# Performance work log

Measured on AMD Instinct MI355X. Metric: run time of the kernel, lower is better.

The kernel has to match this reference:

```python
import jax, jax.numpy as jnp
import numpy as np

DIM = 768
HEADS = 12
HEAD_DIM = DIM // HEADS
SCALE = HEAD_DIM ** -0.5


def setup_inputs() -> dict:
    key = jax.random.key(0)
    k_x, k_qkv, k_ow, k_ob = jax.random.split(key, 4)
    B, N = 8, 1024
    x = jax.random.normal(k_x, (B, N, DIM), dtype=jnp.float32)
    # nn.Linear weights: out = x @ W.T + b; store torch-layout [out, in]
    w_qkv = jax.random.normal(k_qkv, (3 * DIM, DIM), dtype=jnp.float32) * (DIM ** -0.5)
    w_out = jax.random.normal(k_ow, (DIM, DIM), dtype=jnp.float32) * (DIM ** -0.5)
    b_out = jax.random.normal(k_ob, (DIM,), dtype=jnp.float32) * 0.01
    return {"x": x, "w_qkv": w_qkv, "w_out": w_out, "b_out": b_out}


def reference(x, w_qkv, w_out, b_out):
    B, N, C = x.shape
    qkv = jnp.einsum('bnc,dc->bnd', x, w_qkv)            # [B, N, 3C]
    qkv = qkv.reshape(B, N, 3, HEADS, HEAD_DIM)
    qkv = jnp.transpose(qkv, (2, 0, 3, 1, 4))            # [3, B, H, N, Dh]
    q, k, v = qkv[0], qkv[1], qkv[2]
    attn = jnp.einsum('bhqd,bhkd->bhqk', q, k) * SCALE   # [B, H, N, N]
    attn = jax.nn.softmax(attn, axis=-1)
    o = jnp.einsum('bhqk,bhkd->bhqd', attn, v)           # [B, H, N, Dh]
    o = jnp.transpose(o, (0, 2, 1, 3)).reshape(B, N, C)
    return jnp.einsum('bnc,dc->bnd', o, w_out) + b_out
```

## Files before the change

### kernel.cpp

```cpp
#include <hip/hip_runtime.h>

#define B_ 8
#define N_ 1024
#define DIM_ 768
#define H_ 12
#define DH_ 64
#define M_ (B_ * N_)
#define NQKV_ (3 * DIM_)
#define SCL_ 0.18033688011112042f

typedef unsigned short u16;
typedef unsigned int u32;
typedef __attribute__((ext_vector_type(8))) unsigned short u16x8;
typedef __attribute__((ext_vector_type(4))) unsigned short u16x4;
typedef __attribute__((ext_vector_type(8))) short bf16x8;
typedef __attribute__((ext_vector_type(4))) float f32x4;

__device__ __forceinline__ u16 f2bf(float f) {
  u32 u = __builtin_bit_cast(u32, f);
  u += 0x7fffu + ((u >> 16) & 1u);
  return (u16)(u >> 16);
}
__device__ __forceinline__ float bf2f(u16 v) {
  u32 u = ((u32)v) << 16;
  return __builtin_bit_cast(float, u);
}
__device__ __forceinline__ void async16(const void* g, void* l) {
  __builtin_amdgcn_global_load_lds(
      (const __attribute__((address_space(1))) unsigned int*)g,
      (__attribute__((address_space(3))) unsigned int*)l, 16, 0, 0);
}

__global__ __launch_bounds__(256) void cast_bf16_k(const float* __restrict__ in,
                                                   u16* __restrict__ out, int n4) {
  int i = blockIdx.x * 256 + threadIdx.x;
  if (i >= n4) return;
  float4 v = reinterpret_cast<const float4*>(in)[i];
  u16x4 o;
  o.x = f2bf(v.x); o.y = f2bf(v.y); o.z = f2bf(v.z); o.w = f2bf(v.w);
  reinterpret_cast<u16x4*>(out)[i] = o;
}

template <bool OUT_BF16, bool BIAS, bool VSPLIT>
__global__ __launch_bounds__(256) void gemm_bt_k(
    const u16* __restrict__ A, const u16* __restrict__ Bm,
    void* __restrict__ Cv, const float* __restrict__ bias, int K, int ldc,
    u16* __restrict__ vT) {
  __shared__ u16 As[128 * 32];
  __shared__ u16 Bs[128 * 32];
  const int t = threadIdx.x;
  const int lane = t & 63;
  const int wid = t >> 6;
  const int brow = blockIdx.y << 7;
  const int bcol = blockIdx.x << 7;
  const int wrow = (wid >> 1) << 6;
  const int wcol = (wid & 1) << 6;

  f32x4 acc[4][4];
#pragma unroll
  for (int m = 0; m < 4; ++m)
#pragma unroll
    for (int n = 0; n < 4; ++n) acc[m][n] = (f32x4){0.f, 0.f, 0.f, 0.f};

  const int loff0 = t << 4, loff1 = (t + 256) << 4;
  const int r0 = loff0 >> 6, r1 = loff1 >> 6;
  const int s0 = ((((loff0 >> 4) & 3) ^ (r0 & 3)) << 3);
  const int s1 = ((((loff1 >> 4) & 3) ^ (r1 & 3)) << 3);
  const u16* gA0 = A + (size_t)(brow + r0) * K + s0;
  const u16* gA1 = A + (size_t)(brow + r1) * K + s1;
  const u16* gB0 = Bm + (size_t)(bcol + r0) * K + s0;
  const u16* gB1 = Bm + (size_t)(bcol + r1) * K + s1;
  char* lA = (char*)As;
  char* lB = (char*)Bs;

  const int kb = (lane >> 4) << 4;
  int aoff[4], boff[4];
#pragma unroll
  for (int m = 0; m < 4; ++m) {
    int ra = wrow + (m << 4) + (lane & 15);
    aoff[m] = (ra << 6) + (kb ^ ((ra & 3) << 4));
    int rb = wcol + (m << 4) + (lane & 15);
    boff[m] = (rb << 6) + (kb ^ ((rb & 3) << 4));
  }

  const int nkt = K >> 5;
  for (int kt = 0; kt < nkt; ++kt) {
    const int ko = kt << 5;
    async16(gA0 + ko, lA + loff0);
    async16(gA1 + ko, lA + loff1);
    async16(gB0 + ko, lB + loff0);
    async16(gB1 + ko, lB + loff1);
    __syncthreads();
    bf16x8 af[4], bfr[4];
#pragma unroll
    for (int m = 0; m < 4; ++m) af[m] = *(const bf16x8*)(lA + aoff[m]);
#pragma unroll
    for (int n = 0; n < 4; ++n) bfr[n] = *(const bf16x8*)(lB + boff[n]);
#pragma unroll
    for (int m = 0; m < 4; ++m)
#pragma unroll
      for (int n = 0; n < 4; ++n)
        acc[m][n] = __builtin_amdgcn_mfma_f32_16x16x32_bf16(af[m], bfr[n],
                                                            acc[m][n], 0, 0, 0);
    __syncthreads();
  }

  const int crow = brow + wrow + ((lane >> 4) << 2);
  const int ccol0 = bcol + wcol + (lane & 15);
  if (VSPLIT && bcol >= 2 * DIM_) {
#pragma unroll
    for (int n = 0; n < 4; ++n) {
      int colh = ccol0 + (n << 4) - 2 * DIM_;
      int h = colh >> 6, d = colh & 63;
#pragma unroll
      for (int m = 0; m < 4; ++m) {
        int row0 = crow + (m << 4);
        int bb = row0 >> 10, nn = row0 & 1023;
        int hbl = bb * H_ + h;
        uint2 pk;
        pk.x = (u32)f2bf(acc[m][n][0]) | ((u32)f2bf(acc[m][n][1]) << 16);
        pk.y = (u32)f2bf(acc[m][n][2]) | ((u32)f2bf(acc[m][n][3]) << 16);
        *(uint2*)(vT + (((size_t)(hbl * 64 + d)) << 10) + nn) = pk;
      }
    }
    return;
  }
#pragma unroll
  for (int m = 0; m < 4; ++m)
#pragma unroll
    for (int n = 0; n < 4; ++n) {
      int col = ccol0 + (n << 4);
      float bv = BIAS ? bias[col] : 0.f;
#pragma unroll
      for (int j = 0; j < 4; ++j) {
        int row = crow + (m << 4) + j;
        if (OUT_BF16)
          ((u16*)Cv)[(size_t)row * ldc + col] = f2bf(acc[m][n][j]);
        else
          ((float*)Cv)[(size_t)row * ldc + col] = acc[m][n][j] + bv;
      }
    }
}

__global__ __launch_bounds__(256) void attn_k(const u16* __restrict__ qkv,
                                              const u16* __restrict__ vT,
                                              u16* __restrict__ ob) {
  __shared__ u16 Ks[64 * 64];
  __shared__ u16 Vt[64 * 64];
  __shared__ u16 Ps[4][16 * 64];
  const int t = threadIdx.x;
  const int lane = t & 63;
  const int w = t >> 6;
  const int g = lane >> 4;
  const int q15 = lane & 15;

  const int orig = blockIdx.x;
  const int sub = orig >> 3;
  const int hb = (orig & 7) * 12 + (sub >> 4);
  const int qt = sub & 15;
  const int b = hb / H_;
  const int h = hb - b * H_;
  const int rowbase = b * N_;
  const int qcol = h * DH_;
  const int kcol = DIM_ + qcol;

  bf16x8 qf[2];
  {
    const int qrow = rowbase + (qt << 6) + (w << 4) + q15;
    const u16* src = qkv + (size_t)qrow * NQKV_ + qcol + (g << 3);
#pragma unroll
    for (int ks = 0; ks < 2; ++ks) {
      u16x8 raw = *(const u16x8*)(src + ks * 32);
      bf16x8 o;
#pragma unroll
      for (int j = 0; j < 8; ++j) o[j] = (short)f2bf(bf2f(raw[j]) * SCL_);
      qf[ks] = o;
    }
  }

  float mrow = -1e30f, lrow = 0.f;
  f32x4 oacc[4];
#pragma unroll
  for (int d = 0; d < 4; ++d) oacc[d] = (f32x4){0.f, 0.f, 0.f, 0.f};

  const int sr = t >> 3;
  const int c8 = t & 7;
  const int loff0 = t << 4, loff1 = (t + 256) << 4;
  const u16* kg0 = qkv + (size_t)(rowbase + sr) * NQKV_ + kcol + ((c8 ^ (sr & 7)) << 3);
  const u16* kg1 = qkv + (size_t)(rowbase + sr + 32) * NQKV_ + kcol + ((c8 ^ (sr & 7)) << 3);
  const u16* vg0 = vT + (((size_t)(hb * 64 + sr)) << 10) + ((c8 ^ (sr & 7)) << 3);
  const u16* vg1 = vT + (((size_t)(hb * 64 + sr + 32)) << 10) + ((c8 ^ (sr & 7)) << 3);
  char* lk = (char*)Ks;
  char* lv = (char*)Vt;
  char* lp = (char*)&Ps[w][0];

  for (int kv = 0; kv < 16; ++kv) {
    __syncthreads();
    async16(kg0 + (size_t)kv * 64 * NQKV_, lk + loff0);
    async16(kg1 + (size_t)kv * 64 * NQKV_, lk + loff1);
    async16(vg0 + kv * 64, lv + loff0);
    async16(vg1 + kv * 64, lv + loff1);
    __syncthreads();

    f32x4 s[4];
#pragma unroll
    for (int n = 0; n < 4; ++n) s[n] = (f32x4){0.f, 0.f, 0.f, 0.f};
#pragma unroll
    for (int n = 0; n < 4; ++n) {
      int rk = (n << 4) + q15;
#pragma unroll
      for (int ks = 0; ks < 2; ++ks) {
        int off = (rk << 7) + (((ks << 6) + (g << 4)) ^ ((rk & 7) << 4));
        bf16x8 kf = *(const bf16x8*)(lk + off);
        s[n] = __builtin_amdgcn_mfma_f32_16x16x32_bf16(kf, qf[ks], s[n], 0, 0, 0);
      }
    }

    float mx = s[0][0];
#pragma unroll
    for (int n = 0; n < 4; ++n)
#pragma unroll
      for (int j = 0; j < 4; ++j) mx = fmaxf(mx, s[n][j]);
    mx = fmaxf(mx, __shfl_xor(mx, 16, 64));
    mx = fmaxf(mx, __shfl_xor(mx, 32, 64));
    float mn = fmaxf(mrow, mx);
    float al = exp2f(mrow - mn);
    mrow = mn;
    float p[4][4];
    float ps = 0.f;
#pragma unroll
    for (int n = 0; n < 4; ++n)
#pragma unroll
      for (int j = 0; j < 4; ++j) {
        p[n][j] = exp2f(s[n][j] - mn);
        ps += p[n][j];
      }
    ps += __shfl_xor(ps, 16, 64);
    ps += __shfl_xor(ps, 32, 64);
    lrow = lrow * al + ps;

    float alj[4];
#pragma unroll
    for (int j = 0; j < 4; ++j) alj[j] = __shfl(al, (g << 2) + j, 64);
#pragma unroll
    for (int d = 0; d < 4; ++d)
#pragma unroll
      for (int j = 0; j < 4; ++j) oacc[d][j] *= alj[j];

#pragma unroll
    for (int n = 0; n < 4; ++n) {
      uint2 pk;
      pk.x = (u32)f2bf(p[n][0]) | ((u32)f2bf(p[n][1]) << 16);
      pk.y = (u32)f2bf(p[n][2]) | ((u32)f2bf(p[n][3]) << 16);
      *(uint2*)(lp + (q15 << 7) + (((n << 5) + (g << 3)) ^ ((q15 & 7) << 4))) = pk;
    }

    bf16x8 pf[2];
#pragma unroll
    for (int ks = 0; ks < 2; ++ks)
      pf[ks] = *(const bf16x8*)(lp + (q15 << 7) +
                                (((ks << 6) + (g << 4)) ^ ((q15 & 7) << 4)));
#pragma unroll
    for (int dt = 0; dt < 4; ++dt) {
      int d = (dt << 4) + q15;
#pragma unroll
      for (int ks = 0; ks < 2; ++ks) {
        bf16x8 vf = *(const bf16x8*)(lv + (d << 7) +
                                     (((ks << 6) + (g << 4)) ^ ((d & 7) << 4)));
        oacc[dt] = __builtin_amdgcn_mfma_f32_16x16x32_bf16(pf[ks], vf, oacc[dt], 0, 0, 0);
      }
    }
  }

  float rl = 1.f / lrow;
  float rlj[4];
#pragma unroll
  for (int j = 0; j < 4; ++j) rlj[j] = __shfl(rl, (g << 2) + j, 64);
  const int orow0 = rowbase + (qt << 6) + (w << 4) + (g << 2);
#pragma unroll
  for (int dt = 0; dt < 4; ++dt) {
    int col = qcol + (dt << 4) + q15;
#pragma unroll
    for (int j = 0; j < 4; ++j)
      ob[(size_t)(orow0 + j) * DIM_ + col] = f2bf(oacc[dt][j] * rlj[j]);
  }
}

extern "C" void kernel_launch(void* const* d_in, const int* in_sizes, int n_in,
                              void* d_out, int out_size, void* d_ws, size_t ws_size,
                              hipStream_t stream) {
  const float* x = (const float*)d_in[0];
  const float* w_qkv = (const float*)d_in[1];
  const float* w_out = (const float*)d_in[2];
  const float* b_out = (const float*)d_in[3];

  u16* xb = (u16*)d_ws;
  u16* wqkvb = xb + (size_t)M_ * DIM_;
  u16* woutb = wqkvb + (size_t)NQKV_ * DIM_;
  u16* qkvb = woutb + (size_t)DIM_ * DIM_;
  u16* obuf = qkvb + (size_t)M_ * NQKV_;
  u16* vT = obuf + (size_t)M_ * DIM_;

  {
    int n4 = M_ * DIM_ / 4;
    cast_bf16_k<<<(n4 + 255) / 256, 256, 0, stream>>>(x, xb, n4);
  }
  {
    int n4 = NQKV_ * DIM_ / 4;
    cast_bf16_k<<<(n4 + 255) / 256, 256, 0, stream>>>(w_qkv, wqkvb, n4);
  }
  {
    int n4 = DIM_ * DIM_ / 4;
    cast_bf16_k<<<(n4 + 255) / 256, 256, 0, stream>>>(w_out, woutb, n4);
  }

  gemm_bt_k<true, false, true><<<dim3(NQKV_ / 128, M_ / 128), 256, 0, stream>>>(
      xb, wqkvb, (void*)qkvb, nullptr, DIM_, NQKV_, vT);

  attn_k<<<dim3(B_ * H_ * 16), 256, 0, stream>>>(qkvb, vT, obuf);

  gemm_bt_k<false, true, false><<<dim3(DIM_ / 128, M_ / 128), 256, 0, stream>>>(
      obuf, woutb, d_out, b_out, DIM_, DIM_, nullptr);
}
```

Baseline: 228.7 us.

## Double-buffer K/V tiles in attention and add lazy softmax rescaling

The attention kernel now double-buffers the K and V tiles in LDS, issuing the async loads for tile kv+1 before computing on tile kv so global latency overlaps with MFMA work. One barrier per iteration replaces the previous two. It also skips the online-softmax rescale of the accumulator unless the running max grows by more than 8 (log2 domain), and switches to the raw exp2 builtin, packed bf16 conversion and s_setprio hints around MFMA blocks. The costs are doubled LDS for K/V, which may lower occupancy, and that probabilities can reach up to 2^8 before rescaling, which changes rounding slightly.

```diff
diff --git a/kernel.cpp b/kernel.cpp
--- a/kernel.cpp
+++ b/kernel.cpp
@@ -24,6 +24,11 @@
 __device__ __forceinline__ float bf2f(u16 v) {
   u32 u = ((u32)v) << 16;
   return __builtin_bit_cast(float, u);
+}
+__device__ __forceinline__ u32 cvtpk_bf16(float lo, float hi) {
+  u32 r;
+  asm("v_cvt_pk_bf16_f32 %0, %1, %2" : "=v"(r) : "v"(lo), "v"(hi));
+  return r;
 }
 __device__ __forceinline__ void async16(const void* g, void* l) {
   __builtin_amdgcn_global_load_lds(
@@ -145,8 +150,8 @@
 __global__ __launch_bounds__(256) void attn_k(const u16* __restrict__ qkv,
                                               const u16* __restrict__ vT,
                                               u16* __restrict__ ob) {
-  __shared__ u16 Ks[64 * 64];
-  __shared__ u16 Vt[64 * 64];
+  __shared__ u16 Ks[2][64 * 64];
+  __shared__ u16 Vt[2][64 * 64];
   __shared__ u16 Ps[4][16 * 64];
   const int t = threadIdx.x;
   const int lane = t & 63;
@@ -190,86 +195,108 @@
   const u16* kg1 = qkv + (size_t)(rowbase + sr + 32) * NQKV_ + kcol + ((c8 ^ (sr & 7)) << 3);
   const u16* vg0 = vT + (((size_t)(hb * 64 + sr)) << 10) + ((c8 ^ (sr & 7)) << 3);
   const u16* vg1 = vT + (((size_t)(hb * 64 + sr + 32)) << 10) + ((c8 ^ (sr & 7)) << 3);
-  char* lk = (char*)Ks;
-  char* lv = (char*)Vt;
-  char* lp = (char*)&Ps[w][0];
+  char* lk0 = (char*)Ks;
+  char* lv0 = (char*)Vt;
+  char* lp = (char*)Ps + (w << 11);
+
+  const int rowB = q15 << 7;
+  const int xsw = (q15 & 7) << 4;
+  const int x0 = (g << 4) ^ xsw;
+  const int x1 = (64 + (g << 4)) ^ xsw;
+
+  async16(kg0, lk0 + loff0);
+  async16(kg1, lk0 + loff1);
+  async16(vg0, lv0 + loff0);
+  async16(vg1, lv0 + loff1);
+  asm volatile("s_waitcnt vmcnt(0)" ::: "memory");
+  __builtin_amdgcn_s_barrier();
 
   for (int kv = 0; kv < 16; ++kv) {
-    __syncthreads();
-    async16(kg0 + (size_t)kv * 64 * NQKV_, lk + loff0);
-    async16(kg1 + (size_t)kv * 64 * NQKV_, lk + loff1);
-    async16(vg0 + kv * 64, lv + loff0);
-    async16(vg1 + kv * 64, lv + loff1);
-    __syncthreads();
-
-    f32x4 s[4];
-#pragma unroll
-    for (int n = 0; n < 4; ++n) s[n] = (f32x4){0.f, 0.f, 0.f, 0.f};
+    const int cur = kv & 1;
+    if (kv < 15) {
+      const int nb = (cur ^ 1) << 13;
+      const size_t kofs = (size_t)(kv + 1) * 64;
+      async16(kg0 + kofs * NQKV_, lk0 + nb + loff0);
+      async16(kg1 + kofs * NQKV_, lk0 + nb + loff1);
+      async16(vg0 + kofs, lv0 + nb + loff0);
+      async16(vg1 + kofs, lv0 + nb + loff1);
+    }
+    const char* lkc = lk0 + (cur << 13);
+    const char* lvc = lv0 + (cur << 13);
+
+    f32x4 s4[4];
+#pragma unroll
+    for (int n = 0; n < 4; ++n) s4[n] = (f32x4){0.f, 0.f, 0.f, 0.f};
+    __builtin_amdgcn_s_setprio(1);
 #pragma unroll
     for (int n = 0; n < 4; ++n) {
-      int rk = (n << 4) + q15;
-#pragma unroll
-      for (int ks = 0; ks < 2; ++ks) {
-        int off = (rk << 7) + (((ks << 6) + (g << 4)) ^ ((rk & 7) << 4));
-        bf16x8 kf = *(const bf16x8*)(lk + off);
-        s[n] = __builtin_amdgcn_mfma_f32_16x16x32_bf16(kf, qf[ks], s[n], 0, 0, 0);
-      }
-    }
-
-    float mx = s[0][0];
-#pragma unroll
-    for (int n = 0; n < 4; ++n)
-#pragma unroll
-      for (int j = 0; j < 4; ++j) mx = fmaxf(mx, s[n][j]);
-    mx = fmaxf(mx, __shfl_xor(mx, 16, 64));
-    mx = fmaxf(mx, __shfl_xor(mx, 32, 64));
-    float mn = fmaxf(mrow, mx);
-    float al = exp2f(mrow - mn);
-    mrow = mn;
+      bf16x8 kf0 = *(const bf16x8*)(lkc + (n << 11) + rowB + x0);
+      s4[n] = __builtin_amdgcn_mfma_f32_16x16x32_bf16(kf0, qf[0], s4[n], 0, 0, 0);
+      bf16x8 kf1 = *(const bf16x8*)(lkc + (n << 11) + rowB + x1);
+      s4[n] = __builtin_amdgcn_mfma_f32_16x16x32_bf16(kf1, qf[1], s4[n], 0, 0, 0);
+    }
+    __builtin_amdgcn_s_setprio(0);
+
+    float mx;
+    {
+      float a0 = fmaxf(fmaxf(s4[0][0], s4[0][1]), fmaxf(s4[0][2], s4[0][3]));
+      float a1 = fmaxf(fmaxf(s4[1][0], s4[1][1]), fmaxf(s4[1][2], s4[1][3]));
+      float a2 = fmaxf(fmaxf(s4[2][0], s4[2][1]), fmaxf(s4[2][2], s4[2][3]));
+      float a3 = fmaxf(fmaxf(s4[3][0], s4[3][1]), fmaxf(s4[3][2], s4[3][3]));
+      mx = fmaxf(fmaxf(a0, a1), fmaxf(a2, a3));
+      mx = fmaxf(mx, __shfl_xor(mx, 16, 64));
+      mx = fmaxf(mx, __shfl_xor(mx, 32, 64));
+    }
+    if (!__all(mx - mrow <= 8.f)) {
+      float mn = fmaxf(mrow, mx);
+      float al = __builtin_amdgcn_exp2f(mrow - mn);
+      mrow = mn;
+      lrow *= al;
+      float alj[4];
+#pragma unroll
+      for (int j = 0; j < 4; ++j) alj[j] = __shfl(al, (g << 2) + j, 64);
+#pragma unroll
+      for (int d = 0; d < 4; ++d)
+#pragma unroll
+        for (int j = 0; j < 4; ++j) oacc[d][j] *= alj[j];
+    }
+
     float p[4][4];
     float ps = 0.f;
 #pragma unroll
     for (int n = 0; n < 4; ++n)
 #pragma unroll
       for (int j = 0; j < 4; ++j) {
-        p[n][j] = exp2f(s[n][j] - mn);
+        p[n][j] = __builtin_amdgcn_exp2f(s4[n][j] - mrow);
         ps += p[n][j];
       }
     ps += __shfl_xor(ps, 16, 64);
     ps += __shfl_xor(ps, 32, 64);
-    lrow = lrow * al + ps;
-
-    float alj[4];
-#pragma unroll
-    for (int j = 0; j < 4; ++j) alj[j] = __shfl(al, (g << 2) + j, 64);
-#pragma unroll
-    for (int d = 0; d < 4; ++d)
-#pragma unroll
-      for (int j = 0; j < 4; ++j) oacc[d][j] *= alj[j];
+    lrow += ps;
 
 #pragma unroll
     for (int n = 0; n < 4; ++n) {
       uint2 pk;
-      pk.x = (u32)f2bf(p[n][0]) | ((u32)f2bf(p[n][1]) << 16);
-      pk.y = (u32)f2bf(p[n][2]) | ((u32)f2bf(p[n][3]) << 16);
-      *(uint2*)(lp + (q15 << 7) + (((n << 5) + (g << 3)) ^ ((q15 & 7) << 4))) = pk;
-    }
-
-    bf16x8 pf[2];
-#pragma unroll
-    for (int ks = 0; ks < 2; ++ks)
-      pf[ks] = *(const bf16x8*)(lp + (q15 << 7) +
-                                (((ks << 6) + (g << 4)) ^ ((q15 & 7) << 4)));
+      pk.x = cvtpk_bf16(p[n][0], p[n][1]);
+      pk.y = cvtpk_bf16(p[n][2], p[n][3]);
+      *(uint2*)(lp + rowB + (((n << 5) + (g << 3)) ^ xsw)) = pk;
+    }
+
+    bf16x8 pf0 = *(const bf16x8*)(lp + rowB + x0);
+    bf16x8 pf1 = *(const bf16x8*)(lp + rowB + x1);
+    __builtin_amdgcn_s_setprio(1);
 #pragma unroll
     for (int dt = 0; dt < 4; ++dt) {
-      int d = (dt << 4) + q15;
-#pragma unroll
-      for (int ks = 0; ks < 2; ++ks) {
-        bf16x8 vf = *(const bf16x8*)(lv + (d << 7) +
-                                     (((ks << 6) + (g << 4)) ^ ((d & 7) << 4)));
-        oacc[dt] = __builtin_amdgcn_mfma_f32_16x16x32_bf16(pf[ks], vf, oacc[dt], 0, 0, 0);
-      }
-    }
+      bf16x8 vf0 = *(const bf16x8*)(lvc + (dt << 11) + rowB + x0);
+      oacc[dt] = __builtin_amdgcn_mfma_f32_16x16x32_bf16(pf0, vf0, oacc[dt], 0, 0, 0);
+      bf16x8 vf1 = *(const bf16x8*)(lvc + (dt << 11) + rowB + x1);
+      oacc[dt] = __builtin_amdgcn_mfma_f32_16x16x32_bf16(pf1, vf1, oacc[dt], 0, 0, 0);
+    }
+    __builtin_amdgcn_s_setprio(0);
+
+    asm volatile("s_waitcnt vmcnt(0)" ::: "memory");
+    __builtin_amdgcn_s_barrier();
+    __builtin_amdgcn_sched_barrier(0);
   }
 
   float rl = 1.f / lrow;
```

Result: faster. 213.2 us (-6.8%).
